# Kernel tuning notes

Hardware: AMD Instinct MI355X
Metric: run time of the kernel (lower is better)

## Reference

```python
import jax, jax.numpy as jnp
import numpy as np
jax.config.update('jax_enable_x64', True)

T = 524288      # hash table size (2^19)
D = 3           # input_dim
F = 2           # feature_dim
L = 16          # levels
N_MIN, N_MAX = 16, 512
B = 262144      # batch of query points
V = 2 ** D      # voxel corners

_b = np.exp((np.log(N_MAX) - np.log(N_MIN)) / (L - 1))
RESOLUTIONS = jnp.asarray(np.floor(N_MIN * _b ** np.arange(L)).astype(np.int64)).reshape(1, 1, L, 1)
PRIMES = jnp.asarray(np.array([1, 2654435761, 805459861], dtype=np.int64))
_border = np.empty((D, V), dtype=np.int64)
for i in range(D):
    _border[i, :] = np.array(([0] * 2 ** i + [1] * 2 ** i) * 2 ** (D - i - 1), dtype=np.int64)
BORDER_ADDS = jnp.asarray(_border).reshape(1, D, 1, V)


def setup_inputs() -> dict:
    key = jax.random.key(0)
    kx, kt = jax.random.split(key)
    x = jax.random.uniform(kx, (B, D), dtype=jnp.float32)  # coords in [0,1)
    # nn.Embedding init: uniform(-1e-4, 1e-4) per level
    tables = jax.random.uniform(kt, (L, T, F), dtype=jnp.float32, minval=-1e-4, maxval=1e-4)
    return {"x": x, "tables": tables}


def reference(x, tables):
    # scale to each grid resolution: (B, D, L, 1)
    scaled = x[:, :, None, None] * RESOLUTIONS.astype(x.dtype)
    # voxel corner integer coords: (B, D, L, V)
    grid = jnp.floor(scaled).astype(jnp.int64) + BORDER_ADDS
    # NVIDIA fast hash: xor of coord*prime over dims, mod T -> (B, L, V)
    hashed = grid * PRIMES.reshape(1, D, 1, 1)
    idx = jnp.remainder(jnp.bitwise_xor(jnp.bitwise_xor(hashed[:, 0], hashed[:, 1]), hashed[:, 2]), T)
    # gather per-level features: (B, L, V, F)
    feats = tables[jnp.arange(L)[None, :, None], idx]
    # multilinear interpolation weights: prod over dims -> (B, L, V)
    w = jnp.prod(1.0 - jnp.abs(scaled - grid.astype(scaled.dtype)), axis=1)
    # weighted corner sum -> (B, L, F) -> (B, L*F)
    out = jnp.einsum('blv,blvf->blf', w, feats)
    return out.reshape(x.shape[0], L * F)
```

## Files before the change

kernel.cpp:

```cpp
#include <hip/hip_runtime.h>


constexpr int      kT      = 524288;
constexpr unsigned kMask   = kT - 1;
constexpr int      kB      = 262144;
constexpr unsigned kP1     = 2654435761u;
constexpr unsigned kP2     = 805459861u;
constexpr int      kBins   = 4096;
constexpr int      kCap    = 128;
constexpr int      kOvfCap = 65536;
constexpr int      kCoopTot = 845;

typedef float f32x4 __attribute__((ext_vector_type(4)));
typedef float f32x2 __attribute__((ext_vector_type(2)));

__device__ __forceinline__ unsigned morton12(float x0, float x1, float x2) {
    unsigned a = min(15u, (unsigned)(x0 * 16.0f));
    unsigned b = min(15u, (unsigned)(x1 * 16.0f));
    unsigned c = min(15u, (unsigned)(x2 * 16.0f));
    unsigned key = 0;
#pragma unroll
    for (int i = 3; i >= 0; --i)
        key = (key << 3) | (((a >> i) & 1u) << 2) | (((b >> i) & 1u) << 1) | ((c >> i) & 1u);
    return key;
}

__device__ __forceinline__ f32x2 direct_level(const float x0, const float x1, const float x2,
                                              const float res,
                                              const f32x4* __restrict__ tab4) {
    const float s0 = x0 * res, s1 = x1 * res, s2 = x2 * res;
    const float f0 = floorf(s0), f1 = floorf(s1), f2 = floorf(s2);
    const float r0 = s0 - f0, r1 = s1 - f1, r2 = s2 - f2;
    const unsigned c0 = (unsigned)f0;
    const unsigned h1a = (unsigned)f1 * kP1, h1b = h1a + kP1;
    const unsigned h2a = (unsigned)f2 * kP2, h2b = h2a + kP2;
    const float w0a = 1.0f - r0, w1a = 1.0f - r1, w2a = 1.0f - r2;
    float a0 = 0.0f, a1 = 0.0f;
#pragma unroll
    for (int q = 0; q < 4; ++q) {
        const unsigned g = ((q & 1) ? h1b : h1a) ^ ((q & 2) ? h2b : h2a);
        const unsigned i0 = (c0 ^ g) & kMask;
        const unsigned i1 = ((c0 + 1u) ^ g) & kMask;
        const f32x4 A = tab4[i0 >> 1];
        const f32x4 B = tab4[i1 >> 1];
        const float p0x = (i0 & 1) ? A.z : A.x;
        const float p0y = (i0 & 1) ? A.w : A.y;
        const float p1x = (i1 & 1) ? B.z : B.x;
        const float p1y = (i1 & 1) ? B.w : B.y;
        const float wyz = ((q & 1) ? r1 : w1a) * ((q & 2) ? r2 : w2a);
        const float wl = wyz * w0a;
        const float wr = wyz * r0;
        a0 = fmaf(wl, p0x, fmaf(wr, p1x, a0));
        a1 = fmaf(wl, p0y, fmaf(wr, p1y, a1));
    }
    f32x2 r; r.x = a0; r.y = a1;
    return r;
}

__device__ __forceinline__ void hashenc_body(const float x0, const float x1, const float x2,
                                             const f32x4* __restrict__ tab4base,
                                             f32x4* __restrict__ out, const unsigned sid) {
    f32x4 o[8];
    constexpr float kResF[16] = {16, 20, 25, 32, 40, 50, 64, 80,
                                 101, 128, 161, 203, 256, 322, 406, 512};
#pragma unroll
    for (int l = 0; l < 16; ++l) {
        const f32x2 r = direct_level(x0, x1, x2, kResF[l], tab4base + (size_t)l * (kT / 2));
        if (l & 1) { o[l >> 1].z = r.x; o[l >> 1].w = r.y; }
        else       { o[l >> 1].x = r.x; o[l >> 1].y = r.y; }
    }
    f32x4* op = out + (size_t)sid * 8;
#pragma unroll
    for (int k = 0; k < 8; ++k) __builtin_nontemporal_store(o[k], op + k);
}

template <int L, int N, int RES, int OFF>
__device__ __forceinline__ void coop_fill(const unsigned lane,
                                          const unsigned bx, const unsigned by, const unsigned bz,
                                          const f32x2* __restrict__ tab2,
                                          f32x2* __restrict__ wlds) {
    const unsigned lo0 = (bx * RES) >> 4, lo1 = (by * RES) >> 4, lo2 = (bz * RES) >> 4;
    const unsigned h1 = lo1 * kP1, h2 = lo2 * kP2;
    constexpr int NC = N * N * N;
#pragma unroll
    for (int k = 0; k < (NC + 63) / 64; ++k) {
        const int t = (int)lane + 64 * k;
        if (t < NC) {
            const unsigned dx = (unsigned)t / (N * N);
            const unsigned rem = (unsigned)t % (N * N);
            const unsigned dy = rem / N, dz = rem % N;
            const unsigned idx = ((lo0 + dx) ^ (h1 + dy * kP1) ^ (h2 + dz * kP2)) & kMask;
            wlds[OFF + t] = tab2[(size_t)L * kT + idx];
        }
    }
}

template <int N, int RES, int OFF>
__device__ __forceinline__ f32x2 coop_interp(const float x0, const float x1, const float x2,
                                             const unsigned bx, const unsigned by, const unsigned bz,
                                             const f32x2* __restrict__ wlds) {
    const float res = (float)RES;
    const float s0 = x0 * res, s1 = x1 * res, s2 = x2 * res;
    const float f0 = floorf(s0), f1 = floorf(s1), f2 = floorf(s2);
    const float r0 = s0 - f0, r1 = s1 - f1, r2 = s2 - f2;
    const unsigned lo0 = (bx * RES) >> 4, lo1 = (by * RES) >> 4, lo2 = (bz * RES) >> 4;
    const unsigned i0 = min((unsigned)f0 - lo0, (unsigned)(N - 2));
    const unsigned i1 = min((unsigned)f1 - lo1, (unsigned)(N - 2));
    const unsigned i2 = min((unsigned)f2 - lo2, (unsigned)(N - 2));
    const int s00 = OFF + (int)(i0 * (N * N) + i1 * N + i2);
    const f32x2 c000 = wlds[s00],             c001 = wlds[s00 + 1];
    const f32x2 c010 = wlds[s00 + N],         c011 = wlds[s00 + N + 1];
    const f32x2 c100 = wlds[s00 + N * N],     c101 = wlds[s00 + N * N + 1];
    const f32x2 c110 = wlds[s00 + N * N + N], c111 = wlds[s00 + N * N + N + 1];
    const float w0a = 1.f - r0, w1a = 1.f - r1, w2a = 1.f - r2;
    const float w00 = w0a * w1a, w01 = w0a * r1, w10 = r0 * w1a, w11 = r0 * r1;
    float a0 = w00 * w2a * c000.x;
    float a1 = w00 * w2a * c000.y;
    a0 = fmaf(w00 * r2,  c001.x, a0); a1 = fmaf(w00 * r2,  c001.y, a1);
    a0 = fmaf(w01 * w2a, c010.x, a0); a1 = fmaf(w01 * w2a, c010.y, a1);
    a0 = fmaf(w01 * r2,  c011.x, a0); a1 = fmaf(w01 * r2,  c011.y, a1);
    a0 = fmaf(w10 * w2a, c100.x, a0); a1 = fmaf(w10 * w2a, c100.y, a1);
    a0 = fmaf(w10 * r2,  c101.x, a0); a1 = fmaf(w10 * r2,  c101.y, a1);
    a0 = fmaf(w11 * w2a, c110.x, a0); a1 = fmaf(w11 * w2a, c110.y, a1);
    a0 = fmaf(w11 * r2,  c111.x, a0); a1 = fmaf(w11 * r2,  c111.y, a1);
    f32x2 r; r.x = a0; r.y = a1;
    return r;
}

__global__ __launch_bounds__(256) void scatter_kernel(const float* __restrict__ x,
                                                      unsigned* __restrict__ cnt,
                                                      f32x4* __restrict__ xsort,
                                                      f32x4* __restrict__ ovf) {
    const int i = blockIdx.x * 256 + threadIdx.x;
    const float x0 = x[3 * i], x1 = x[3 * i + 1], x2 = x[3 * i + 2];
    const unsigned key = morton12(x0, x1, x2);
    const unsigned slot = atomicAdd(&cnt[key], 1u);
    f32x4 v;
    v.x = x0; v.y = x1; v.z = x2; v.w = __uint_as_float((unsigned)i);
    if (slot < (unsigned)kCap) {
        xsort[key * kCap + slot] = v;
    } else {
        const unsigned o = atomicAdd(&cnt[kBins], 1u);
        if (o < (unsigned)kOvfCap) ovf[o] = v;
    }
}

__global__ __launch_bounds__(256, 6) void hashenc_main(const f32x4* __restrict__ xsort,
                                                       const unsigned* __restrict__ cnt,
                                                       const f32x2* __restrict__ tab2,
                                                       const f32x4* __restrict__ tab4base,
                                                       f32x4* __restrict__ out) {
    __shared__ f32x2 lds[4][kCoopTot];
    const int tid = threadIdx.x;
    const int bid = (int)((blockIdx.x & 7) * 256 + (blockIdx.x >> 3));
    const int gs  = bid * 256 + tid;
    const int bin = gs >> 7;
    const int sl  = gs & (kCap - 1);
    const unsigned n = min(cnt[bin], (unsigned)kCap);
    if ((unsigned)(sl & 64) >= n) return;
    const bool valid = (unsigned)sl < n;
    const f32x4 v = xsort[gs];
    const float x0 = valid ? v.x : 0.5f;
    const float x1 = valid ? v.y : 0.5f;
    const float x2 = valid ? v.z : 0.5f;

    const unsigned key = (unsigned)bin;
    const unsigned bx = ((key >> 2) & 1) | ((key >> 4) & 2) | ((key >> 6) & 4) | ((key >> 8) & 8);
    const unsigned by = ((key >> 1) & 1) | ((key >> 3) & 2) | ((key >> 5) & 4) | ((key >> 7) & 8);
    const unsigned bz = ((key     ) & 1) | ((key >> 2) & 2) | ((key >> 4) & 4) | ((key >> 6) & 8);

    f32x2* wlds = lds[tid >> 6];
    const unsigned lane = (unsigned)(tid & 63);

    coop_fill<0, 2, 16,   0>(lane, bx, by, bz, tab2, wlds);
    coop_fill<1, 4, 20,   8>(lane, bx, by, bz, tab2, wlds);
    coop_fill<2, 4, 25,  72>(lane, bx, by, bz, tab2, wlds);
    coop_fill<3, 3, 32, 136>(lane, bx, by, bz, tab2, wlds);
    coop_fill<4, 5, 40, 163>(lane, bx, by, bz, tab2, wlds);
    coop_fill<5, 6, 50, 288>(lane, bx, by, bz, tab2, wlds);
    coop_fill<6, 5, 64, 504>(lane, bx, by, bz, tab2, wlds);
    coop_fill<7, 6, 80, 629>(lane, bx, by, bz, tab2, wlds);

    f32x4 o0, o1, o2, o3;
    { const f32x2 r = coop_interp<2, 16,   0>(x0, x1, x2, bx, by, bz, wlds); o0.x = r.x; o0.y = r.y; }
    { const f32x2 r = coop_interp<4, 20,   8>(x0, x1, x2, bx, by, bz, wlds); o0.z = r.x; o0.w = r.y; }
    { const f32x2 r = coop_interp<4, 25,  72>(x0, x1, x2, bx, by, bz, wlds); o1.x = r.x; o1.y = r.y; }
    { const f32x2 r = coop_interp<3, 32, 136>(x0, x1, x2, bx, by, bz, wlds); o1.z = r.x; o1.w = r.y; }
    { const f32x2 r = coop_interp<5, 40, 163>(x0, x1, x2, bx, by, bz, wlds); o2.x = r.x; o2.y = r.y; }
    { const f32x2 r = coop_interp<6, 50, 288>(x0, x1, x2, bx, by, bz, wlds); o2.z = r.x; o2.w = r.y; }
    { const f32x2 r = coop_interp<5, 64, 504>(x0, x1, x2, bx, by, bz, wlds); o3.x = r.x; o3.y = r.y; }
    { const f32x2 r = coop_interp<6, 80, 629>(x0, x1, x2, bx, by, bz, wlds); o3.z = r.x; o3.w = r.y; }

    if (valid) {
        constexpr float kResF[8] = {101, 128, 161, 203, 256, 322, 406, 512};
        f32x4 o[4];
#pragma unroll
        for (int j = 0; j < 8; ++j) {
            const int l = 8 + j;
            const f32x2 r = direct_level(x0, x1, x2, kResF[j], tab4base + (size_t)l * (kT / 2));
            if (j & 1) { o[j >> 1].z = r.x; o[j >> 1].w = r.y; }
            else       { o[j >> 1].x = r.x; o[j >> 1].y = r.y; }
        }
        f32x4* op = out + (size_t)__float_as_uint(v.w) * 8;
        __builtin_nontemporal_store(o0, op + 0);
        __builtin_nontemporal_store(o1, op + 1);
        __builtin_nontemporal_store(o2, op + 2);
        __builtin_nontemporal_store(o3, op + 3);
#pragma unroll
        for (int k = 0; k < 4; ++k) __builtin_nontemporal_store(o[k], op + 4 + k);
    }
}

__global__ __launch_bounds__(256) void cleanup_kernel(const f32x4* __restrict__ ovf,
                                                      const unsigned* __restrict__ cnt,
                                                      const f32x4* __restrict__ tab4base,
                                                      f32x4* __restrict__ out) {
    const unsigned oc = min(cnt[kBins], (unsigned)kOvfCap);
    for (unsigned j = threadIdx.x; j < oc; j += 256) {
        const f32x4 v = ovf[j];
        hashenc_body(v.x, v.y, v.z, tab4base, out, __float_as_uint(v.w));
    }
}

__global__ __launch_bounds__(256, 4) void hashenc_direct(const float* __restrict__ x,
                                                         const f32x4* __restrict__ tab4base,
                                                         f32x4* __restrict__ out) {
    const int i = blockIdx.x * 256 + threadIdx.x;
    hashenc_body(x[3 * i], x[3 * i + 1], x[3 * i + 2], tab4base, out, (unsigned)i);
}

extern "C" void kernel_launch(void* const* d_in, const int* in_sizes, int n_in,
                              void* d_out, int out_size, void* d_ws, size_t ws_size,
                              hipStream_t stream) {
    const float*  x    = (const float*)d_in[0];
    const f32x2*  tab2 = (const f32x2*)d_in[1];
    const f32x4*  tab4 = (const f32x4*)d_in[1];
    f32x4*        out  = (f32x4*)d_out;

    const size_t cntBytes   = (size_t)(kBins + 16) * 4;
    const size_t ovfBytes   = (size_t)kOvfCap * 16;
    const size_t xsortBytes = (size_t)kBins * kCap * 16;
    const size_t need = cntBytes + ovfBytes + xsortBytes;

    if (ws_size >= need) {
        unsigned* cnt   = (unsigned*)d_ws;
        f32x4*    ovf   = (f32x4*)((char*)d_ws + cntBytes);
        f32x4*    xsort = ovf + kOvfCap;
        hipMemsetAsync(cnt, 0, cntBytes, stream);
        scatter_kernel<<<kB / 256, 256, 0, stream>>>(x, cnt, xsort, ovf);
        hashenc_main<<<(kBins * kCap) / 256, 256, 0, stream>>>(xsort, cnt, tab2, tab4, out);
        cleanup_kernel<<<1, 256, 0, stream>>>(ovf, cnt, tab4, out);
    } else {
        hashenc_direct<<<kB / 256, 256, 0, stream>>>(x, tab4, out);
    }
}
```

Baseline: 152.1 us.

## Split fine-level lookups into per-level blocks in original point order

```diff
diff --git a/kernel.cpp b/kernel.cpp
--- a/kernel.cpp
+++ b/kernel.cpp
@@ -145,14 +145,38 @@
     }
 }
 
-__global__ __launch_bounds__(256, 6) void hashenc_main(const f32x4* __restrict__ xsort,
+__global__ __launch_bounds__(256, 5) void hashenc_main(const float* __restrict__ x,
+                                                       const f32x4* __restrict__ xsort,
                                                        const unsigned* __restrict__ cnt,
                                                        const f32x2* __restrict__ tab2,
                                                        const f32x4* __restrict__ tab4base,
                                                        f32x4* __restrict__ out) {
     __shared__ f32x2 lds[4][kCoopTot];
     const int tid = threadIdx.x;
-    const int bid = (int)((blockIdx.x & 7) * 256 + (blockIdx.x >> 3));
+    const int b = (int)blockIdx.x;
+
+    if (b < 2048) {
+        constexpr float kFineRes[8] = {101, 128, 161, 203, 256, 322, 406, 512};
+        const int j = b & 7;
+        const int chunk = b >> 3;
+        const float res = kFineRes[j];
+        const f32x4* __restrict__ tab4 = tab4base + (size_t)(8 + j) * (kT / 2);
+        f32x2* __restrict__ out2 = (f32x2*)out;
+        const int sbase = chunk * 1024 + tid;
+#pragma unroll
+        for (int it = 0; it < 4; ++it) {
+            const int s = sbase + 256 * it;
+            const float x0 = x[3 * s + 0];
+            const float x1 = x[3 * s + 1];
+            const float x2 = x[3 * s + 2];
+            const f32x2 r = direct_level(x0, x1, x2, res, tab4);
+            __builtin_nontemporal_store(r, out2 + (size_t)s * 16 + 8 + j);
+        }
+        return;
+    }
+
+    const int c = b - 2048;
+    const int bid = (int)((c & 7) * 256 + (c >> 3));
     const int gs  = bid * 256 + tid;
     const int bin = gs >> 7;
     const int sl  = gs & (kCap - 1);
@@ -192,22 +216,11 @@
     { const f32x2 r = coop_interp<6, 80, 629>(x0, x1, x2, bx, by, bz, wlds); o3.z = r.x; o3.w = r.y; }
 
     if (valid) {
-        constexpr float kResF[8] = {101, 128, 161, 203, 256, 322, 406, 512};
-        f32x4 o[4];
-#pragma unroll
-        for (int j = 0; j < 8; ++j) {
-            const int l = 8 + j;
-            const f32x2 r = direct_level(x0, x1, x2, kResF[j], tab4base + (size_t)l * (kT / 2));
-            if (j & 1) { o[j >> 1].z = r.x; o[j >> 1].w = r.y; }
-            else       { o[j >> 1].x = r.x; o[j >> 1].y = r.y; }
-        }
         f32x4* op = out + (size_t)__float_as_uint(v.w) * 8;
         __builtin_nontemporal_store(o0, op + 0);
         __builtin_nontemporal_store(o1, op + 1);
         __builtin_nontemporal_store(o2, op + 2);
         __builtin_nontemporal_store(o3, op + 3);
-#pragma unroll
-        for (int k = 0; k < 4; ++k) __builtin_nontemporal_store(o[k], op + 4 + k);
     }
 }
 
@@ -248,7 +261,7 @@
         f32x4*    xsort = ovf + kOvfCap;
         hipMemsetAsync(cnt, 0, cntBytes, stream);
         scatter_kernel<<<kB / 256, 256, 0, stream>>>(x, cnt, xsort, ovf);
-        hashenc_main<<<(kBins * kCap) / 256, 256, 0, stream>>>(xsort, cnt, tab2, tab4, out);
+        hashenc_main<<<4096, 256, 0, stream>>>(x, xsort, cnt, tab2, tab4, out);
         cleanup_kernel<<<1, 256, 0, stream>>>(ovf, cnt, tab4, out);
     } else {
         hashenc_direct<<<kB / 256, 256, 0, stream>>>(x, tab4, out);
```

New measurement: 138.5 us. 1.1x faster.
